# Optimization experiments

Measured on AMD Instinct MI355X. Metric: run time of the kernel, lower is better.

Reference implementation:

```python
import jax, jax.numpy as jnp
import numpy as np

EMBED_DIM = 1024
SHIFT = 0.0

def setup_inputs() -> dict:
    key = jax.random.key(0)
    k1, k2, k3 = jax.random.split(key, 3)
    inputs = jax.random.normal(k1, (4, 2048, EMBED_DIM), dtype=jnp.float32)
    rotation_params = jax.random.normal(k2, (EMBED_DIM, EMBED_DIM), dtype=jnp.float32)
    entangle_params = jax.random.normal(k3, (EMBED_DIM, EMBED_DIM), dtype=jnp.float32)
    return {"inputs": inputs, "rotation_params": rotation_params, "entangle_params": entangle_params}

def reference(inputs, rotation_params, entangle_params):
    # inputs: (b, s, d)
    d = inputs.shape[-1]
    query = jnp.einsum('bsd,de->bse', inputs, rotation_params)
    key = jnp.einsum('bsd,de->bse', inputs, entangle_params)
    scores = jax.nn.softmax(jnp.einsum('bqd,bkd->bqk', query, key) / np.sqrt(d), axis=-1)
    out = jnp.einsum('bqk,bkd->bqd', scores, inputs)
    return jax.nn.sigmoid(out + SHIFT)
```

## Files before the change

### kernel.cpp

```cpp
#include <hip/hip_runtime.h>
#include <hip/hip_bf16.h>
#include <math.h>


using u16 = unsigned short;
using short8 = __attribute__((ext_vector_type(8))) short;
using f32x4  = __attribute__((ext_vector_type(4))) float;

#define MFB(a, b, c) __builtin_amdgcn_mfma_f32_16x16x32_bf16((a), (b), (c), 0, 0, 0)

__device__ static inline u16 f2bf(float f) {
    union { __hip_bfloat16 h; u16 u; } cv; cv.h = __float2bfloat16(f); return cv.u;
}
__device__ static inline float bf2f(u16 u) {
    union { __hip_bfloat16 h; u16 u; } cv; cv.u = u; return __bfloat162float(cv.h);
}
__device__ static inline void split2(float v, u16& h, u16& l) {
    h = f2bf(v);
    l = f2bf(v - bf2f(h));
}

__device__ static inline void gload16(const u16* g, u16* l) {
    __builtin_amdgcn_global_load_lds(
        (const __attribute__((address_space(1))) void*)g,
        (__attribute__((address_space(3))) void*)l, 16, 0, 0);
}

__device__ static inline short8 ldfrag(const u16* sm, int row, int g) {
    const int off = row * 32 + ((g ^ ((row >> 1) & 3)) << 3);
    return *reinterpret_cast<const short8*>(sm + off);
}

enum { EP_F32 = 0, EP_HILO = 1, EP_SIG = 2 };

template<int EPI, bool TRIPLE, int KH>
__global__ __launch_bounds__(256)
void gemm_split(const u16* __restrict__ Ahi, const u16* __restrict__ Alo,
                const u16* __restrict__ Bhi, const u16* __restrict__ Blo,
                float* __restrict__ Cf, u16* __restrict__ Chi, u16* __restrict__ Clo,
                int K, int lda, int ldb, int ldc,
                long sA, long sB, long sC, float alpha)
{
    const int z = blockIdx.z;
    Ahi += z * sA;
    Bhi += z * sB;
    if (TRIPLE) { Alo += z * sA; Blo += z * sB; }
    if (EPI == EP_HILO) { Chi += z * sC; Clo += z * sC; }
    else                { Cf  += z * sC; }

    constexpr int AUNIT = TRIPLE ? 8192 : 4096;
    constexpr int BUFSZ = KH * 2 * AUNIT;
    __shared__ __align__(16) u16 smem[2 * BUFSZ];

    const int t = threadIdx.x;
    const int wave = t >> 6, lane = t & 63;
    const int row0 = blockIdx.y * 128, col0 = blockIdx.x * 128;

    const int rr = t >> 2, cc = t & 3;
    const int gg = cc ^ ((rr >> 1) & 3);
    const u16* gAh = Ahi + (long)(row0 + rr) * lda + gg * 8;
    const u16* gBh = Bhi + (long)(col0 + rr) * ldb + gg * 8;
    const u16* gAl = TRIPLE ? (Alo + (long)(row0 + rr) * lda + gg * 8) : nullptr;
    const u16* gBl = TRIPLE ? (Blo + (long)(col0 + rr) * ldb + gg * 8) : nullptr;
    const long a2 = (long)64 * lda, b2 = (long)64 * ldb;

    auto STAGE = [&](int buf, int k0) {
        u16* base = smem + buf * BUFSZ + t * 8;
        #pragma unroll
        for (int kh = 0; kh < KH; kh++) {
            const int kk = k0 + kh * 32;
            u16* dA = base + kh * AUNIT;
            u16* dB = base + KH * AUNIT + kh * AUNIT;
            gload16(gAh + kk,      dA);
            gload16(gAh + kk + a2, dA + 2048);
            gload16(gBh + kk,      dB);
            gload16(gBh + kk + b2, dB + 2048);
            if (TRIPLE) {
                gload16(gAl + kk,      dA + 4096);
                gload16(gAl + kk + a2, dA + 6144);
                gload16(gBl + kk,      dB + 4096);
                gload16(gBl + kk + b2, dB + 6144);
            }
        }
    };

    f32x4 acc[4][4];
    #pragma unroll
    for (int m = 0; m < 4; m++)
        #pragma unroll
        for (int n = 0; n < 4; n++)
            acc[m][n] = (f32x4){0.f, 0.f, 0.f, 0.f};

    const int lr = lane & 15, lg = lane >> 4;
    const int wm = (wave >> 1) * 64, wn = (wave & 1) * 64;
    const int NT = K / (32 * KH);

    STAGE(0, 0);

    for (int tk = 0; tk < NT; ++tk) {
        __syncthreads();
        const u16* sb = smem + (tk & 1) * BUFSZ;
        if (tk + 1 < NT) STAGE((tk + 1) & 1, (tk + 1) * 32 * KH);

        #pragma unroll
        for (int kh = 0; kh < KH; kh++) {
            const u16* sAh = sb + kh * AUNIT;
            const u16* sAl = sAh + 4096;
            const u16* sBh = sb + KH * AUNIT + kh * AUNIT;
            const u16* sBl = sBh + 4096;

            short8 bh[4], bl[4], ah[4], al[4];
            #pragma unroll
            for (int n = 0; n < 4; n++) {
                bh[n] = ldfrag(sBh, wn + n * 16 + lr, lg);
                if (TRIPLE) bl[n] = ldfrag(sBl, wn + n * 16 + lr, lg);
            }
            #pragma unroll
            for (int m = 0; m < 4; m++) {
                ah[m] = ldfrag(sAh, wm + m * 16 + lr, lg);
                if (TRIPLE) al[m] = ldfrag(sAl, wm + m * 16 + lr, lg);
            }
            __builtin_amdgcn_s_setprio(1);
            #pragma unroll
            for (int m = 0; m < 4; m++) {
                #pragma unroll
                for (int n = 0; n < 4; n++) {
                    acc[m][n] = MFB(ah[m], bh[n], acc[m][n]);
                    if (TRIPLE) {
                        acc[m][n] = MFB(ah[m], bl[n], acc[m][n]);
                        acc[m][n] = MFB(al[m], bh[n], acc[m][n]);
                    }
                }
            }
            __builtin_amdgcn_s_setprio(0);
        }
    }

    #pragma unroll
    for (int m = 0; m < 4; m++) {
        #pragma unroll
        for (int n = 0; n < 4; n++) {
            #pragma unroll
            for (int r = 0; r < 4; r++) {
                const int grow = row0 + wm + m * 16 + lg * 4 + r;
                const int gcol = col0 + wn + n * 16 + lr;
                const float v = alpha * acc[m][n][r];
                const long o = (long)grow * ldc + gcol;
                if (EPI == EP_F32) {
                    Cf[o] = v;
                } else if (EPI == EP_SIG) {
                    Cf[o] = 1.0f / (1.0f + __expf(-v));
                } else {
                    u16 h, l; split2(v, h, l);
                    Chi[o] = h; Clo[o] = l;
                }
            }
        }
    }
}

__global__ __launch_bounds__(1024)
void gemm_triple_256(const u16* __restrict__ Ahi, const u16* __restrict__ Alo,
                     const u16* __restrict__ Bhi, const u16* __restrict__ Blo,
                     float* __restrict__ Cf,
                     int K, int lda, int ldb, int ldc,
                     long sA, long sB, long sC, float alpha)
{
    const int z = blockIdx.z;
    Ahi += z * sA; Alo += z * sA;
    Bhi += z * sB; Blo += z * sB;
    Cf  += z * sC;

    __shared__ __align__(16) u16 smem[65536];

    const int t = threadIdx.x;
    const int wave = t >> 6, lane = t & 63;
    const int lr = lane & 15, lg = lane >> 4;

    const int u = blockIdx.x + 8 * blockIdx.y;
    const int reg = u & 7, j = u >> 3;
    const int bx = 2 * (reg & 3) + (j & 1);
    const int by = 4 * (reg >> 2) + (j >> 1);
    const int row0 = by * 256, col0 = bx * 256;
    const int wm = (wave >> 2) * 64, wn = (wave & 3) * 64;

    const int srow = t >> 2;
    const int sg = (t & 3) ^ ((srow >> 1) & 3);
    const u16* gAh = Ahi + (long)(row0 + srow) * lda + sg * 8;
    const u16* gAl = Alo + (long)(row0 + srow) * lda + sg * 8;
    const u16* gBh = Bhi + (long)(col0 + srow) * ldb + sg * 8;
    const u16* gBl = Blo + (long)(col0 + srow) * ldb + sg * 8;

    f32x4 acc[4][4];
    #pragma unroll
    for (int m = 0; m < 4; m++)
        #pragma unroll
        for (int n = 0; n < 4; n++)
            acc[m][n] = (f32x4){0.f, 0.f, 0.f, 0.f};

    const int NT = K >> 5;

    {
        u16* d = smem + t * 8;
        gload16(gAh, d);
        gload16(gAl, d + 8192);
        gload16(gBh, d + 16384);
        gload16(gBl, d + 24576);
    }

    for (int tk = 0; tk < NT; ++tk) {
        __syncthreads();
        const u16* sb = smem + (tk & 1) * 32768;
        if (tk + 1 < NT) {
            const int kn = (tk + 1) << 5;
            u16* d = smem + ((tk + 1) & 1) * 32768 + t * 8;
            gload16(gAh + kn, d);
            gload16(gAl + kn, d + 8192);
            gload16(gBh + kn, d + 16384);
            gload16(gBl + kn, d + 24576);
        }
        const u16* sAh = sb;
        const u16* sAl = sb + 8192;
        const u16* sBh = sb + 16384;
        const u16* sBl = sb + 24576;

        short8 bh[4], bl[4];
        #pragma unroll
        for (int n = 0; n < 4; n++) {
            bh[n] = ldfrag(sBh, wn + n * 16 + lr, lg);
            bl[n] = ldfrag(sBl, wn + n * 16 + lr, lg);
        }
        __builtin_amdgcn_s_setprio(1);
        #pragma unroll
        for (int m = 0; m < 4; m++) {
            const short8 ah = ldfrag(sAh, wm + m * 16 + lr, lg);
            const short8 al = ldfrag(sAl, wm + m * 16 + lr, lg);
            #pragma unroll
            for (int n = 0; n < 4; n++) {
                acc[m][n] = MFB(ah, bh[n], acc[m][n]);
                acc[m][n] = MFB(ah, bl[n], acc[m][n]);
                acc[m][n] = MFB(al, bh[n], acc[m][n]);
            }
        }
        __builtin_amdgcn_s_setprio(0);
    }

    #pragma unroll
    for (int m = 0; m < 4; m++) {
        #pragma unroll
        for (int n = 0; n < 4; n++) {
            #pragma unroll
            for (int r = 0; r < 4; r++) {
                const int grow = row0 + wm + m * 16 + lg * 4 + r;
                const int gcol = col0 + wn + n * 16 + lr;
                Cf[(long)grow * ldc + gcol] = alpha * acc[m][n][r];
            }
        }
    }
}

__global__ __launch_bounds__(256)
void split_rm3(const float* __restrict__ in0, u16* __restrict__ hi0, u16* __restrict__ lo0, long n0,
               const float* __restrict__ in1, u16* __restrict__ hi1, u16* __restrict__ lo1, long n1,
               const float* __restrict__ in2, u16* __restrict__ hi2, u16* __restrict__ lo2)
{
    long i = ((long)blockIdx.x * 256 + threadIdx.x) * 4;
    const float* in; u16 *hi, *lo;
    if (i < n0)           { in = in0; hi = hi0; lo = lo0; }
    else if (i < n0 + n1) { i -= n0; in = in1; hi = hi1; lo = lo1; }
    else                  { i -= n0 + n1; in = in2; hi = hi2; lo = lo2; }
    const float4 v = *reinterpret_cast<const float4*>(in + i);
    ushort4 h, l;
    split2(v.x, h.x, l.x);
    split2(v.y, h.y, l.y);
    split2(v.z, h.z, l.z);
    split2(v.w, h.w, l.w);
    *reinterpret_cast<ushort4*>(hi + i) = h;
    *reinterpret_cast<ushort4*>(lo + i) = l;
}

__global__ __launch_bounds__(256)
void reduce4_split(const float* __restrict__ p, u16* __restrict__ hi, u16* __restrict__ lo,
                   long n)
{
    const long i = ((long)blockIdx.x * 256 + threadIdx.x) * 4;
    const float4 a = *reinterpret_cast<const float4*>(p + i);
    const float4 b = *reinterpret_cast<const float4*>(p + n + i);
    const float4 c = *reinterpret_cast<const float4*>(p + 2 * n + i);
    const float4 d = *reinterpret_cast<const float4*>(p + 3 * n + i);
    ushort4 h, l;
    split2((a.x + b.x) + (c.x + d.x), h.x, l.x);
    split2((a.y + b.y) + (c.y + d.y), h.y, l.y);
    split2((a.z + b.z) + (c.z + d.z), h.z, l.z);
    split2((a.w + b.w) + (c.w + d.w), h.w, l.w);
    *reinterpret_cast<ushort4*>(hi + i) = h;
    *reinterpret_cast<ushort4*>(lo + i) = l;
}

template<bool HILO>
__global__ __launch_bounds__(256)
void split_tr(const float* __restrict__ in, u16* __restrict__ hi, u16* __restrict__ lo,
              int R, int C, long sIn, long sOut)
{
    in += (long)blockIdx.z * sIn;
    hi += (long)blockIdx.z * sOut;
    if (HILO) lo += (long)blockIdx.z * sOut;

    __shared__ float tile[32][33];
    const int tx = threadIdx.x & 31, ty = threadIdx.x >> 5;
    const int r0 = blockIdx.y * 32, c0 = blockIdx.x * 32;

    #pragma unroll
    for (int j = 0; j < 4; j++)
        tile[ty * 4 + j][tx] = in[(long)(r0 + ty * 4 + j) * C + c0 + tx];
    __syncthreads();

    #pragma unroll
    for (int j = 0; j < 4; j++) {
        const int oc = ty * 4 + j;
        const float v = tile[tx][oc];
        u16 h, l; split2(v, h, l);
        const long o = (long)(c0 + oc) * R + r0 + tx;
        hi[o] = h;
        if (HILO) lo[o] = l;
    }
}

__global__ __launch_bounds__(256)
void softmax_hi(const float* __restrict__ S, u16* __restrict__ hi)
{
    const int NC = 2048;
    const long base = (long)blockIdx.x * NC;
    const float* p = S + base;
    const int tid = threadIdx.x;

    float4 v0 = reinterpret_cast<const float4*>(p)[tid];
    float4 v1 = reinterpret_cast<const float4*>(p)[tid + 256];

    float m = fmaxf(fmaxf(fmaxf(v0.x, v0.y), fmaxf(v0.z, v0.w)),
                    fmaxf(fmaxf(v1.x, v1.y), fmaxf(v1.z, v1.w)));
    #pragma unroll
    for (int off = 1; off < 64; off <<= 1)
        m = fmaxf(m, __shfl_xor(m, off));

    __shared__ float redm[4];
    __shared__ float reds[4];
    const int wave = tid >> 6, lane = tid & 63;
    if (lane == 0) redm[wave] = m;
    __syncthreads();
    m = fmaxf(fmaxf(redm[0], redm[1]), fmaxf(redm[2], redm[3]));

    v0.x = __expf(v0.x - m); v0.y = __expf(v0.y - m);
    v0.z = __expf(v0.z - m); v0.w = __expf(v0.w - m);
    v1.x = __expf(v1.x - m); v1.y = __expf(v1.y - m);
    v1.z = __expf(v1.z - m); v1.w = __expf(v1.w - m);

    float s = (v0.x + v0.y + v0.z + v0.w) + (v1.x + v1.y + v1.z + v1.w);
    #pragma unroll
    for (int off = 1; off < 64; off <<= 1)
        s += __shfl_xor(s, off);
    if (lane == 0) reds[wave] = s;
    __syncthreads();
    s = (reds[0] + reds[1]) + (reds[2] + reds[3]);

    const float inv = 1.0f / s;
    ushort4 h0, h1;
    h0.x = f2bf(v0.x * inv); h0.y = f2bf(v0.y * inv);
    h0.z = f2bf(v0.z * inv); h0.w = f2bf(v0.w * inv);
    h1.x = f2bf(v1.x * inv); h1.y = f2bf(v1.y * inv);
    h1.z = f2bf(v1.z * inv); h1.w = f2bf(v1.w * inv);

    reinterpret_cast<ushort4*>(hi + base)[tid]       = h0;
    reinterpret_cast<ushort4*>(hi + base)[tid + 256] = h1;
}

extern "C" void kernel_launch(void* const* d_in, const int* in_sizes, int n_in,
                              void* d_out, int out_size, void* d_ws, size_t ws_size,
                              hipStream_t stream)
{
    (void)in_sizes; (void)n_in; (void)out_size; (void)ws_size;
    const float* X = (const float*)d_in[0];
    const float* R = (const float*)d_in[1];
    const float* E = (const float*)d_in[2];
    float* out = (float*)d_out;

    const int B = 4, SQ = 2048, D = 1024;
    const long NDX = (long)B * SQ * D;
    const long DD  = (long)D * D;
    const long SS  = (long)B * SQ * SQ;
    const long M16 = 8388608;

    u16* wsu = (u16*)d_ws;
    u16* Xhi  = wsu;
    u16* Xlo  = Xhi + NDX;
    u16* Rhi  = wsu + 2 * M16;
    u16* Rlo  = Rhi + DD;
    u16* Ehi  = Rlo + DD;
    u16* Elo  = Ehi + DD;
    u16* Yhi  = wsu + 2 * M16;
    u16* Ylo  = Yhi + NDX;
    u16* Shi  = wsu + 2 * M16;
    u16* Xthi = wsu;
    float* Wpart = (float*)(wsu + 4 * M16);
    u16* Wthi = wsu + 5 * M16;
    u16* Wtlo = Wthi + DD;
    float* Sf = (float*)(wsu + 4 * M16);

    dim3 thr(256);

    split_rm3<<<dim3((unsigned)((NDX + 2 * DD) / 1024)), thr, 0, stream>>>(
        X, Xhi, Xlo, NDX, R, Rhi, Rlo, DD, E, Ehi, Elo);

    gemm_split<EP_F32, true, 1><<<dim3(D / 128, D / 128, 4), thr, 0, stream>>>(
        Ehi, Elo, Rhi, Rlo, Wpart, nullptr, nullptr,
        256, D, D, D, 256, 256, DD, 1.0f);
    reduce4_split<<<dim3((unsigned)(DD / 1024)), thr, 0, stream>>>(Wpart, Wthi, Wtlo, DD);

    gemm_split<EP_HILO, true, 1><<<dim3(D / 128, (B * SQ) / 128, 1), thr, 0, stream>>>(
        Xhi, Xlo, Wthi, Wtlo, nullptr, Yhi, Ylo,
        D, D, D, D, 0, 0, 0, 1.0f);

    gemm_triple_256<<<dim3(SQ / 256, SQ / 256, B), dim3(1024), 0, stream>>>(
        Yhi, Ylo, Xhi, Xlo, Sf,
        D, D, D, SQ,
        (long)SQ * D, (long)SQ * D, (long)SQ * SQ, 0.03125f);

    softmax_hi<<<dim3(B * SQ), thr, 0, stream>>>(Sf, Shi);

    split_tr<false><<<dim3(D / 32, SQ / 32, B), thr, 0, stream>>>(
        X, Xthi, nullptr, SQ, D, (long)SQ * D, (long)SQ * D);

    gemm_split<EP_SIG, false, 2><<<dim3(D / 128, SQ / 128, B), thr, 0, stream>>>(
        Shi, nullptr, Xthi, nullptr, out, nullptr, nullptr,
        SQ, SQ, SQ, D,
        (long)SQ * SQ, (long)SQ * D, (long)SQ * D, 1.0f);
}
```

Measured before the change: 240.7 us.

## Add 16-wave 256x128 GEMM kernel for projection and output GEMMs

Adds a new GEMM kernel that uses 1024-thread blocks (16 waves) over a 256x128 output tile with K-step 32, double-buffered LDS loads and swizzled fragments. It replaces the 256-thread 128x128 gemm_split for the X·W projection (triple bf16 split) and for the final scores·X GEMM with the sigmoid epilogue. The goal is more waves per block to hide latency and more reuse of each loaded B tile across rows. In exchange the launch has half as many blocks, and the short K-step means a barrier every 32 elements of K.

After: 246.4 us. +2.4%, slower.

```diff
diff --git a/kernel.cpp b/kernel.cpp
--- a/kernel.cpp
+++ b/kernel.cpp
@@ -140,6 +140,122 @@
     for (int m = 0; m < 4; m++) {
         #pragma unroll
         for (int n = 0; n < 4; n++) {
+            #pragma unroll
+            for (int r = 0; r < 4; r++) {
+                const int grow = row0 + wm + m * 16 + lg * 4 + r;
+                const int gcol = col0 + wn + n * 16 + lr;
+                const float v = alpha * acc[m][n][r];
+                const long o = (long)grow * ldc + gcol;
+                if (EPI == EP_F32) {
+                    Cf[o] = v;
+                } else if (EPI == EP_SIG) {
+                    Cf[o] = 1.0f / (1.0f + __expf(-v));
+                } else {
+                    u16 h, l; split2(v, h, l);
+                    Chi[o] = h; Clo[o] = l;
+                }
+            }
+        }
+    }
+}
+
+template<int EPI, bool TRIPLE>
+__global__ __launch_bounds__(1024)
+void gemm16w(const u16* __restrict__ Ahi, const u16* __restrict__ Alo,
+             const u16* __restrict__ Bhi, const u16* __restrict__ Blo,
+             float* __restrict__ Cf, u16* __restrict__ Chi, u16* __restrict__ Clo,
+             int K, int lda, int ldb, int ldc,
+             long sA, long sB, long sC, float alpha)
+{
+    const int z = blockIdx.z;
+    Ahi += z * sA;
+    Bhi += z * sB;
+    if (TRIPLE) { Alo += z * sA; Blo += z * sB; }
+    if (EPI == EP_HILO) { Chi += z * sC; Clo += z * sC; }
+    else                { Cf  += z * sC; }
+
+    constexpr int ABYTES = 8192;
+    constexpr int BBYTES = 4096;
+    constexpr int BBASE  = TRIPLE ? 16384 : 8192;
+    constexpr int BUFSZ  = TRIPLE ? 24576 : 12288;
+    __shared__ __align__(16) u16 smem[2 * BUFSZ];
+
+    const int t = threadIdx.x;
+    const int wave = t >> 6, lane = t & 63;
+    const int lr = lane & 15, lg = lane >> 4;
+    const int row0 = blockIdx.y * 256, col0 = blockIdx.x * 128;
+    const int wm = (wave >> 2) * 64, wn = (wave & 3) * 32;
+
+    const int ar = t >> 2, ac = t & 3;
+    const int ag = ac ^ ((ar >> 1) & 3);
+    const u16* gAh = Ahi + (long)(row0 + ar) * lda + ag * 8;
+    const u16* gAl = TRIPLE ? (Alo + (long)(row0 + ar) * lda + ag * 8) : nullptr;
+    const int bt = t & 511;
+    const int br = bt >> 2, bc = bt & 3;
+    const int bg = bc ^ ((br >> 1) & 3);
+    const u16* gB = ((t < 512) ? Bhi : Blo) + (long)(col0 + br) * ldb + bg * 8;
+    const int bOff = BBASE + ((t < 512) ? 0 : BBYTES) + bt * 8;
+    const bool doB = TRIPLE || (t < 512);
+
+    f32x4 acc[4][2];
+    #pragma unroll
+    for (int m = 0; m < 4; m++)
+        #pragma unroll
+        for (int n = 0; n < 2; n++)
+            acc[m][n] = (f32x4){0.f, 0.f, 0.f, 0.f};
+
+    const int NT = K >> 5;
+
+    {
+        u16* d = smem + t * 8;
+        gload16(gAh, d);
+        if (TRIPLE) gload16(gAl, d + ABYTES);
+        if (doB) gload16(gB, smem + bOff);
+    }
+
+    for (int tk = 0; tk < NT; ++tk) {
+        __syncthreads();
+        const u16* sb = smem + (tk & 1) * BUFSZ;
+        if (tk + 1 < NT) {
+            const int kn = (tk + 1) << 5;
+            u16* d = smem + ((tk + 1) & 1) * BUFSZ + t * 8;
+            gload16(gAh + kn, d);
+            if (TRIPLE) gload16(gAl + kn, d + ABYTES);
+            if (doB) gload16(gB + kn, smem + ((tk + 1) & 1) * BUFSZ + bOff);
+        }
+        const u16* sAh = sb;
+        const u16* sAl = sb + ABYTES;
+        const u16* sBh = sb + BBASE;
+        const u16* sBl = sBh + BBYTES;
+
+        short8 bh[2], bl[2];
+        #pragma unroll
+        for (int n = 0; n < 2; n++) {
+            bh[n] = ldfrag(sBh, wn + n * 16 + lr, lg);
+            if (TRIPLE) bl[n] = ldfrag(sBl, wn + n * 16 + lr, lg);
+        }
+        __builtin_amdgcn_s_setprio(1);
+        #pragma unroll
+        for (int m = 0; m < 4; m++) {
+            const short8 ah = ldfrag(sAh, wm + m * 16 + lr, lg);
+            short8 al;
+            if (TRIPLE) al = ldfrag(sAl, wm + m * 16 + lr, lg);
+            #pragma unroll
+            for (int n = 0; n < 2; n++) {
+                acc[m][n] = MFB(ah, bh[n], acc[m][n]);
+                if (TRIPLE) {
+                    acc[m][n] = MFB(ah, bl[n], acc[m][n]);
+                    acc[m][n] = MFB(al, bh[n], acc[m][n]);
+                }
+            }
+        }
+        __builtin_amdgcn_s_setprio(0);
+    }
+
+    #pragma unroll
+    for (int m = 0; m < 4; m++) {
+        #pragma unroll
+        for (int n = 0; n < 2; n++) {
             #pragma unroll
             for (int r = 0; r < 4; r++) {
                 const int grow = row0 + wm + m * 16 + lg * 4 + r;
@@ -416,7 +532,7 @@
         256, D, D, D, 256, 256, DD, 1.0f);
     reduce4_split<<<dim3((unsigned)(DD / 1024)), thr, 0, stream>>>(Wpart, Wthi, Wtlo, DD);
 
-    gemm_split<EP_HILO, true, 1><<<dim3(D / 128, (B * SQ) / 128, 1), thr, 0, stream>>>(
+    gemm16w<EP_HILO, true><<<dim3(D / 128, (B * SQ) / 256, 1), dim3(1024), 0, stream>>>(
         Xhi, Xlo, Wthi, Wtlo, nullptr, Yhi, Ylo,
         D, D, D, D, 0, 0, 0, 1.0f);
 
@@ -430,7 +546,7 @@
     split_tr<false><<<dim3(D / 32, SQ / 32, B), thr, 0, stream>>>(
         X, Xthi, nullptr, SQ, D, (long)SQ * D, (long)SQ * D);
 
-    gemm_split<EP_SIG, false, 2><<<dim3(D / 128, SQ / 128, B), thr, 0, stream>>>(
+    gemm16w<EP_SIG, false><<<dim3(D / 128, SQ / 256, B), dim3(1024), 0, stream>>>(
         Shi, nullptr, Xthi, nullptr, out, nullptr, nullptr,
         SQ, SQ, SQ, D,
         (long)SQ * SQ, (long)SQ * D, (long)SQ * D, 1.0f);
```

## Switch triple-bf16 256x256 GEMM to 32x32x16 MFMA with column-major LDS layout

Applied to the files above, without the earlier changes.

Replaces the 16x16x32 bf16 MFMA tiling in the 256-tile triple-split GEMM with 32x32x16 MFMA instructions. Each wave now holds 2x2 32x32 accumulators. The LDS staging layout also changes from a row-swizzled form to a k-group-major layout so each lane reads contiguous 16-byte fragments. The aim is fewer LDS fragment reads per MFMA and higher MFMA throughput. The cost is that the new unswizzled layout may cause LDS bank conflicts and changes the epilogue store pattern.

Measured after the change: 297.0 us. 23.4% more time.

```diff
diff --git a/kernel.cpp b/kernel.cpp
--- a/kernel.cpp
+++ b/kernel.cpp
@@ -6,8 +6,10 @@
 using u16 = unsigned short;
 using short8 = __attribute__((ext_vector_type(8))) short;
 using f32x4  = __attribute__((ext_vector_type(4))) float;
-
-#define MFB(a, b, c) __builtin_amdgcn_mfma_f32_16x16x32_bf16((a), (b), (c), 0, 0, 0)
+using f32x16 = __attribute__((ext_vector_type(16))) float;
+
+#define MFB(a, b, c)   __builtin_amdgcn_mfma_f32_16x16x32_bf16((a), (b), (c), 0, 0, 0)
+#define MFB32(a, b, c) __builtin_amdgcn_mfma_f32_32x32x16_bf16((a), (b), (c), 0, 0, 0)
 
 __device__ static inline u16 f2bf(float f) {
     union { __hip_bfloat16 h; u16 u; } cv; cv.h = __float2bfloat16(f); return cv.u;
@@ -29,6 +31,10 @@
 __device__ static inline short8 ldfrag(const u16* sm, int row, int g) {
     const int off = row * 32 + ((g ^ ((row >> 1) & 3)) << 3);
     return *reinterpret_cast<const short8*>(sm + off);
+}
+
+__device__ static inline short8 ldcol(const u16* sm, int row, int g) {
+    return *reinterpret_cast<const short8*>(sm + g * 2048 + row * 8);
 }
 
 enum { EP_F32 = 0, EP_HILO = 1, EP_SIG = 2 };
@@ -175,7 +181,7 @@
 
     const int t = threadIdx.x;
     const int wave = t >> 6, lane = t & 63;
-    const int lr = lane & 15, lg = lane >> 4;
+    const int l31 = lane & 31, l5 = lane >> 5;
 
     const int u = blockIdx.x + 8 * blockIdx.y;
     const int reg = u & 7, j = u >> 3;
@@ -184,19 +190,20 @@
     const int row0 = by * 256, col0 = bx * 256;
     const int wm = (wave >> 2) * 64, wn = (wave & 3) * 64;
 
-    const int srow = t >> 2;
-    const int sg = (t & 3) ^ ((srow >> 1) & 3);
-    const u16* gAh = Ahi + (long)(row0 + srow) * lda + sg * 8;
-    const u16* gAl = Alo + (long)(row0 + srow) * lda + sg * 8;
-    const u16* gBh = Bhi + (long)(col0 + srow) * ldb + sg * 8;
-    const u16* gBl = Blo + (long)(col0 + srow) * ldb + sg * 8;
-
-    f32x4 acc[4][4];
-    #pragma unroll
-    for (int m = 0; m < 4; m++)
-        #pragma unroll
-        for (int n = 0; n < 4; n++)
-            acc[m][n] = (f32x4){0.f, 0.f, 0.f, 0.f};
+    const int sr = t & 255, sgc = t >> 8;
+    const u16* gAh = Ahi + (long)(row0 + sr) * lda + sgc * 8;
+    const u16* gAl = Alo + (long)(row0 + sr) * lda + sgc * 8;
+    const u16* gBh = Bhi + (long)(col0 + sr) * ldb + sgc * 8;
+    const u16* gBl = Blo + (long)(col0 + sr) * ldb + sgc * 8;
+
+    f32x16 acc[2][2];
+    #pragma unroll
+    for (int m = 0; m < 2; m++)
+        #pragma unroll
+        for (int n = 0; n < 2; n++)
+            #pragma unroll
+            for (int r = 0; r < 16; r++)
+                acc[m][n][r] = 0.f;
 
     const int NT = K >> 5;
 
@@ -224,35 +231,41 @@
         const u16* sBh = sb + 16384;
         const u16* sBl = sb + 24576;
 
-        short8 bh[4], bl[4];
-        #pragma unroll
-        for (int n = 0; n < 4; n++) {
-            bh[n] = ldfrag(sBh, wn + n * 16 + lr, lg);
-            bl[n] = ldfrag(sBl, wn + n * 16 + lr, lg);
-        }
-        __builtin_amdgcn_s_setprio(1);
-        #pragma unroll
-        for (int m = 0; m < 4; m++) {
-            const short8 ah = ldfrag(sAh, wm + m * 16 + lr, lg);
-            const short8 al = ldfrag(sAl, wm + m * 16 + lr, lg);
-            #pragma unroll
-            for (int n = 0; n < 4; n++) {
-                acc[m][n] = MFB(ah, bh[n], acc[m][n]);
-                acc[m][n] = MFB(ah, bl[n], acc[m][n]);
-                acc[m][n] = MFB(al, bh[n], acc[m][n]);
-            }
-        }
-        __builtin_amdgcn_s_setprio(0);
-    }
-
-    #pragma unroll
-    for (int m = 0; m < 4; m++) {
-        #pragma unroll
-        for (int n = 0; n < 4; n++) {
-            #pragma unroll
-            for (int r = 0; r < 4; r++) {
-                const int grow = row0 + wm + m * 16 + lg * 4 + r;
-                const int gcol = col0 + wn + n * 16 + lr;
+        #pragma unroll
+        for (int kk = 0; kk < 2; kk++) {
+            const int g = 2 * kk + l5;
+            short8 bh[2], bl[2], ah[2], al[2];
+            #pragma unroll
+            for (int n = 0; n < 2; n++) {
+                bh[n] = ldcol(sBh, wn + n * 32 + l31, g);
+                bl[n] = ldcol(sBl, wn + n * 32 + l31, g);
+            }
+            #pragma unroll
+            for (int m = 0; m < 2; m++) {
+                ah[m] = ldcol(sAh, wm + m * 32 + l31, g);
+                al[m] = ldcol(sAl, wm + m * 32 + l31, g);
+            }
+            __builtin_amdgcn_s_setprio(1);
+            #pragma unroll
+            for (int m = 0; m < 2; m++)
+                #pragma unroll
+                for (int n = 0; n < 2; n++) {
+                    acc[m][n] = MFB32(ah[m], bh[n], acc[m][n]);
+                    acc[m][n] = MFB32(ah[m], bl[n], acc[m][n]);
+                    acc[m][n] = MFB32(al[m], bh[n], acc[m][n]);
+                }
+            __builtin_amdgcn_s_setprio(0);
+        }
+    }
+
+    #pragma unroll
+    for (int m = 0; m < 2; m++) {
+        #pragma unroll
+        for (int n = 0; n < 2; n++) {
+            #pragma unroll
+            for (int r = 0; r < 16; r++) {
+                const int grow = row0 + wm + m * 32 + (r & 3) + 8 * (r >> 2) + 4 * l5;
+                const int gcol = col0 + wn + n * 32 + l31;
                 Cf[(long)grow * ldc + gcol] = alpha * acc[m][n][r];
             }
         }
```
